# Performance work log

Hardware: AMD Instinct MI355X
Metric: run time of the kernel (lower is better)

Reference implementation:

```python
import jax, jax.numpy as jnp
import numpy as np

B, R, N, D, H, QK, K = 32, 200, 200, 128, 8, 16, 10
CLIP = 10.0  # standard POMO logit clipping


def setup_inputs() -> dict:
    key = jax.random.key(0)
    ks = jax.random.split(key, 12)
    encoded_nodes = jax.random.normal(ks[0], (B, N, D), jnp.float32)
    distance = jax.random.uniform(ks[1], (B, N, N), jnp.float32)
    current = jax.random.randint(ks[2], (B, R), 0, N)
    u = jax.random.uniform(ks[3], (B, R, N))
    ninf_mask = jnp.where(u < 0.3, -jnp.inf, 0.0).astype(jnp.float32)
    s = 0.02
    Wq = jax.random.normal(ks[4], (2 * D, H * QK), jnp.float32) * s
    Wk = jax.random.normal(ks[5], (D, H * QK), jnp.float32) * s
    Wv = jax.random.normal(ks[6], (D, H * QK), jnp.float32) * s
    Wmhc = jax.random.normal(ks[7], (H * QK, D), jnp.float32) * s
    b_mhc = jnp.zeros((D,), jnp.float32)
    W1 = jax.random.normal(ks[8], (K * D, 5 * D), jnp.float32) * s
    b1 = jnp.zeros((5 * D,), jnp.float32)
    W2 = jax.random.normal(ks[9], (5 * D, D), jnp.float32) * s
    b2 = jnp.zeros((D,), jnp.float32)
    return {"encoded_nodes": encoded_nodes, "distance": distance, "ninf_mask": ninf_mask,
            "current": current, "Wq": Wq, "Wk": Wk, "Wv": Wv, "Wmhc": Wmhc, "b_mhc": b_mhc,
            "W1": W1, "b1": b1, "W2": W2, "b2": b2}


def _search_unvisited(current, distance, ninf_mask):
    # rows of distance at current nodes: [B,R,N] (avoids B*R*N*N materialization)
    dist_f = jnp.take_along_axis(distance, current[:, :, None], axis=1)
    dist_m = jnp.where(jnp.isfinite(ninf_mask), dist_f, jnp.inf)
    neg_vals, idx = jax.lax.top_k(-dist_m, K)  # k smallest distances
    vals = -neg_vals
    return jnp.where(jnp.isinf(vals), N, idx)  # pad index N for masked-out slots


def _gather_pad0(encoded_nodes, idx):
    padded = jnp.concatenate([encoded_nodes, jnp.zeros((B, 1, D), encoded_nodes.dtype)], axis=1)
    g = jnp.take_along_axis(padded, idx.reshape(B, R * K)[:, :, None], axis=1)
    return g.reshape(B, R, K, D)


def _gather_pad_avg(a):
    # replace all-zero (pad) rows by the mean of non-zero rows within each [K,D] group
    is_zero = jnp.sum(a, axis=-1) == 0  # [B,R,K]
    cnt = jnp.maximum(jnp.sum(~is_zero, axis=-1).astype(a.dtype), 1e-9)  # [B,R]
    mean = jnp.sum(a, axis=2) / cnt[..., None]  # [B,R,D]
    return jnp.where(is_zero[..., None], mean[:, :, None, :], a)


def reference(encoded_nodes, distance, ninf_mask, current,
              Wq, Wk, Wv, Wmhc, b_mhc, W1, b1, W2, b2):
    knn = _search_unvisited(current, distance, ninf_mask)         # [B,R,K]
    a = _gather_pad0(encoded_nodes, knn)                          # [B,R,K,D]
    b = _gather_pad_avg(a)                                        # [B,R,K,D]
    h = jnp.maximum(b.reshape(B, R, K * D) @ W1 + b1, 0.0)
    unv = h @ W2 + b2                                             # [B,R,D]
    cur_emb = jnp.take_along_axis(encoded_nodes, current[:, :, None], axis=1)  # [B,R,D]
    qin = jnp.concatenate([cur_emb, unv], axis=-1)                # [B,R,2D]
    q = (qin @ Wq).reshape(B, R, H, QK).transpose(0, 2, 1, 3)     # [B,H,R,QK]
    k = (encoded_nodes @ Wk).reshape(B, N, H, QK).transpose(0, 2, 1, 3)
    v = (encoded_nodes @ Wv).reshape(B, N, H, QK).transpose(0, 2, 1, 3)
    score = jnp.einsum('bhrd,bhnd->bhrn', q, k) / jnp.sqrt(jnp.float32(QK))
    score = score + ninf_mask[:, None]                            # [B,H,R,N]
    w = jax.nn.softmax(score, axis=-1)
    out = jnp.einsum('bhrn,bhnd->bhrd', w, v)
    out = out.transpose(0, 2, 1, 3).reshape(B, R, H * QK)
    mh = out @ Wmhc + b_mhc                                       # [B,R,D]
    sh = jnp.einsum('brd,bnd->brn', mh, encoded_nodes) / jnp.sqrt(jnp.float32(D))
    logits = CLIP * jnp.tanh(sh) + ninf_mask
    return jax.nn.softmax(logits, axis=-1)                        # [B,R,N]
```

## Files before the change

kernel.cpp:

```cpp
#include <hip/hip_runtime.h>
#include <hip/hip_bf16.h>
#include <math.h>

#define Bc 32
#define Rc 200
#define Nc 200
#define Dc 128
#define Hc 8
#define QKc 16
#define Kc 10
#define BRc (Bc*Rc)

typedef __attribute__((ext_vector_type(8))) short short8;
typedef __attribute__((ext_vector_type(4))) float f32x4;
typedef unsigned long long u64;

#define GLOAD_LDS16(g, l) __builtin_amdgcn_global_load_lds( \
    (const __attribute__((address_space(1))) void*)(g), \
    (__attribute__((address_space(3))) void*)(l), 16, 0, 0)

__device__ inline void transpose_tile(const float* __restrict__ src, int lds_,
                                      __hip_bfloat16* __restrict__ dst, int ldd,
                                      int k0, int n0, float scale)
{
    __shared__ float tile[32][33];
    int tx = threadIdx.x & 31, ty = threadIdx.x >> 5;
    #pragma unroll
    for (int i = ty; i < 32; i += 8)
        tile[i][tx] = src[(size_t)(k0 + i) * lds_ + n0 + tx];
    __syncthreads();
    #pragma unroll
    for (int i = ty; i < 32; i += 8)
        dst[(size_t)(n0 + i) * ldd + k0 + tx] = __float2bfloat16(tile[tx][i] * scale);
}

__global__ __launch_bounds__(256) void prep_knn_kernel(
    const float* __restrict__ W1, const float* __restrict__ W2,
    const float* __restrict__ Wq, const float* __restrict__ Wmhc,
    const float* __restrict__ Wk, const float* __restrict__ Wv,
    const float* __restrict__ b2, const float* __restrict__ enc,
    const float* __restrict__ dist, const float* __restrict__ mask,
    const int* __restrict__ cur,
    __hip_bfloat16* __restrict__ W1t, __hip_bfloat16* __restrict__ Wkvt,
    __hip_bfloat16* __restrict__ Wmb, __hip_bfloat16* __restrict__ Wcat,
    float* __restrict__ bq, __hip_bfloat16* __restrict__ encb,
    unsigned* __restrict__ aoff, __hip_bfloat16* __restrict__ hq,
    u64* __restrict__ maskbits)
{
    int bid = blockIdx.x;
    int t = threadIdx.x;
    if (bid < 800) {
        transpose_tile(W1, 640, W1t, 1280, (bid % 40) * 32, (bid / 40) * 32, 1.f);
    } else if (bid < 816) {
        int id = bid - 800;
        transpose_tile(Wk, 128, Wkvt, 128, (id & 3) * 32, (id >> 2) * 32, 1.f);
    } else if (bid < 832) {
        int id = bid - 816;
        transpose_tile(Wv, 128, Wkvt + 128 * 128, 128, (id & 3) * 32, (id >> 2) * 32, 1.f);
    } else if (bid < 848) {
        int e = (bid - 832) * 1024 + t * 4;
        #pragma unroll
        for (int j = 0; j < 4; ++j) Wmb[e + j] = __float2bfloat16(Wmhc[e + j]);
    } else if (bid < 864) {
        int id = bid - 848;
        transpose_tile(Wq, 128, Wcat, 768, (id & 3) * 32, (id >> 2) * 32, 0.25f);
    } else if (bid < 904) {
        __shared__ float w2s[16 * 128];
        int j0 = (bid - 864) * 16;
        #pragma unroll
        for (int idx = t; idx < 16 * 128; idx += 256)
            w2s[idx] = W2[(size_t)j0 * 128 + idx];
        __syncthreads();
        int n = t & 127, half = t >> 7;
        float acc[8];
        #pragma unroll
        for (int jj = 0; jj < 8; ++jj) acc[jj] = 0.f;
        const float* wqp = Wq + (size_t)128 * 128 + n;
        #pragma unroll 8
        for (int k = 0; k < 128; ++k) {
            float wq = wqp[(size_t)k * 128];
            #pragma unroll
            for (int jj = 0; jj < 8; ++jj)
                acc[jj] = fmaf(w2s[(half * 8 + jj) * 128 + k], wq, acc[jj]);
        }
        #pragma unroll
        for (int jj = 0; jj < 8; ++jj)
            Wcat[(size_t)n * 768 + 128 + j0 + half * 8 + jj] =
                __float2bfloat16(acc[jj] * 0.25f);
    } else if (bid < 929) {
        size_t base = (size_t)(bid - 904) * 32768 + (size_t)t * 4;
        #pragma unroll 4
        for (int it = 0; it < 32; ++it) {
            size_t i = base + (size_t)it * 1024;
            float4 v = *(const float4*)(enc + i);
            encb[i + 0] = __float2bfloat16(v.x);
            encb[i + 1] = __float2bfloat16(v.y);
            encb[i + 2] = __float2bfloat16(v.z);
            encb[i + 3] = __float2bfloat16(v.w);
        }
    } else if (bid == 929) {
        __shared__ float red[128];
        int n = t & 127, half = t >> 7;
        float a0 = 0.f, a1 = 0.f;
        int kb = half * 64;
        #pragma unroll 8
        for (int k = 0; k < 64; k += 2) {
            a0 = fmaf(b2[kb + k],     Wq[(size_t)(128 + kb + k) * 128 + n], a0);
            a1 = fmaf(b2[kb + k + 1], Wq[(size_t)(128 + kb + k + 1) * 128 + n], a1);
        }
        if (half) red[n] = a0 + a1;
        __syncthreads();
        if (!half) bq[n] = (a0 + a1 + red[n]) * 0.25f;
    } else {
        int lane = t & 63, w = t >> 6;
        int br = (bid - 930) * 4 + w;
        int b = br / Rc;
        int c = cur[br];
        const float* drow = dist + ((size_t)b * Nc + c) * Nc;
        const float* mrow = mask + (size_t)br * Nc;

        float v[4];
        #pragma unroll
        for (int j = 0; j < 4; ++j) {
            int n = lane + 64 * j;
            bool allowed = false;
            float val = INFINITY;
            if (n < Nc) {
                float mv = mrow[n];
                if (!isinf(mv)) { val = drow[n]; allowed = true; }
            }
            v[j] = val;
            u64 wb = __ballot(allowed);
            if (lane == 0) maskbits[(size_t)br * 4 + j] = wb;
        }
        int idxs[Kc];
        unsigned myrow = 0;
        #pragma unroll
        for (int k = 0; k < Kc; ++k) {
            float bv = v[0]; int bn = lane;
            #pragma unroll
            for (int j = 1; j < 4; ++j) {
                if (v[j] < bv) { bv = v[j]; bn = lane + 64 * j; }
            }
            #pragma unroll
            for (int off = 32; off > 0; off >>= 1) {
                float ov = __shfl_xor(bv, off);
                int   on = __shfl_xor(bn, off);
                if (ov < bv || (ov == bv && on < bn)) { bv = ov; bn = on; }
            }
            bool pad = isinf(bv);
            idxs[k] = pad ? Nc : bn;
            if (lane == k) myrow = pad ? (unsigned)(Bc * Nc + br) : (unsigned)(b * Nc + bn);
            int oj = bn >> 6, ol = bn & 63;
            if (!pad && lane == ol) v[oj] = INFINITY;
        }
        if (lane < Kc) aoff[(size_t)br * 16 + lane] = myrow << 7;

        const float* erow = enc + ((size_t)b * Nc + c) * Dc;
        __hip_bfloat16* hrow = hq + (size_t)br * 768;
        hrow[lane]      = __float2bfloat16(erow[lane]);
        hrow[lane + 64] = __float2bfloat16(erow[lane + 64]);

        if (idxs[Kc - 1] == Nc) {
            float cnt = 0.f;
            #pragma unroll
            for (int k = 0; k < Kc; ++k) cnt += (idxs[k] < Nc) ? 1.f : 0.f;
            float icnt = 1.f / fmaxf(cnt, 1e-9f);
            #pragma unroll
            for (int half = 0; half < 2; ++half) {
                int d = lane + 64 * half;
                float sum = 0.f;
                #pragma unroll
                for (int k = 0; k < Kc; ++k) {
                    if (idxs[k] < Nc)
                        sum += enc[((size_t)b * Nc + idxs[k]) * Dc + d];
                }
                encb[((size_t)(Bc * Nc) + br) * Dc + d] = __float2bfloat16(sum * icnt);
            }
        }
    }
}

__global__ __launch_bounds__(256) void fused_gemms_kernel(
    const __hip_bfloat16* __restrict__ encb, const unsigned* __restrict__ aoff,
    const __hip_bfloat16* __restrict__ W1t, const float* __restrict__ b1,
    const __hip_bfloat16* __restrict__ Wkvt, const __hip_bfloat16* __restrict__ Wmb,
    const float* __restrict__ bmhc, const float* __restrict__ enc,
    __hip_bfloat16* __restrict__ hq, __hip_bfloat16* __restrict__ kvf,
    __hip_bfloat16* __restrict__ em, float* __restrict__ be)
{
    __shared__ short Asl[4][64 * 32];
    __shared__ short Bsl[4][64 * 32];
    int bid = blockIdx.x;
    int tid = threadIdx.x;
    int wave = tid >> 6, lane = tid & 63;
    int lrow = lane >> 2;
    int cg   = lane & 3;
    int ss   = (lane >> 3) & 3;
    int gq   = (cg - ss) & 3;
    int wm = wave >> 1, wn = wave & 1;
    int rrow = lane & 15, quad = lane >> 4;
    int srd  = (rrow >> 1) & 3;
    int strip = (wave & 1) * 32;

    if (bid < 1000) {
        int m0 = (bid / 10) * 64, n0 = (bid % 10) * 64;
        unsigned o0[Kc], o1[Kc];
        if (wave < 2) {
            const unsigned* ap0 = aoff + (size_t)(m0 + strip + lrow) * 16;
            const unsigned* ap1 = ap0 + 16 * 16;
            #pragma unroll
            for (int j = 0; j < Kc; ++j) { o0[j] = ap0[j]; o1[j] = ap1[j]; }
        }
        const short* Eb = (const short*)encb;
        const short* gB0 = (const short*)W1t + (size_t)(n0 + strip + lrow) * 1280 + gq * 8;
        const short* gB1 = gB0 + (size_t)16 * 1280;

        f32x4 acc[2][2];
        #pragma unroll
        for (int i = 0; i < 2; ++i)
            #pragma unroll
            for (int j = 0; j < 2; ++j)
                acc[i][j] = (f32x4){0.f, 0.f, 0.f, 0.f};

#define G1_STAGE(bsel, kt) do {                                                   \
            int g_ = (kt) >> 1, hh_ = ((kt) & 1) * 64;                            \
            _Pragma("unroll")                                                     \
            for (int s_ = 0; s_ < 2; ++s_) {                                      \
                if (wave < 2) {                                                   \
                    GLOAD_LDS16(Eb + o0[g_] + hh_ + s_ * 32 + gq * 8,             \
                                &Asl[((bsel) << 1) | s_][strip * 32]);            \
                    GLOAD_LDS16(Eb + o1[g_] + hh_ + s_ * 32 + gq * 8,             \
                                &Asl[((bsel) << 1) | s_][(strip + 16) * 32]);     \
                } else {                                                          \
                    GLOAD_LDS16(gB0 + (kt) * 64 + s_ * 32,                        \
                                &Bsl[((bsel) << 1) | s_][strip * 32]);            \
                    GLOAD_LDS16(gB1 + (kt) * 64 + s_ * 32,                        \
                                &Bsl[((bsel) << 1) | s_][(strip + 16) * 32]);     \
                }                                                                 \
            } } while (0)

#define G1_COMPUTE(bsel) do {                                                     \
            _Pragma("unroll")                                                     \
            for (int s_ = 0; s_ < 2; ++s_) {                                      \
                short8 afr[2], bfr[2];                                            \
                _Pragma("unroll")                                                 \
                for (int mt = 0; mt < 2; ++mt)                                    \
                    afr[mt] = *(const short8*)&Asl[((bsel) << 1) | s_]            \
                        [(wm * 32 + mt * 16 + rrow) * 32 + ((quad + srd) & 3) * 8]; \
                _Pragma("unroll")                                                 \
                for (int nt = 0; nt < 2; ++nt)                                    \
                    bfr[nt] = *(const short8*)&Bsl[((bsel) << 1) | s_]            \
                        [(wn * 32 + nt * 16 + rrow) * 32 + ((quad + srd) & 3) * 8]; \
                _Pragma("unroll")                                                 \
                for (int mt = 0; mt < 2; ++mt)                                    \
                    _Pragma("unroll")                                             \
                    for (int nt = 0; nt < 2; ++nt)                                \
                        acc[mt][nt] = __builtin_amdgcn_mfma_f32_16x16x32_bf16(    \
                            afr[mt], bfr[nt], acc[mt][nt], 0, 0, 0);              \
            } } while (0)

        G1_STAGE(0, 0);
        __syncthreads();
        #pragma unroll
        for (int kt = 0; kt < 19; ++kt) {
            G1_STAGE((kt & 1) ^ 1, kt + 1);
            G1_COMPUTE(kt & 1);
            __syncthreads();
        }
        G1_COMPUTE(1);
#undef G1_STAGE
#undef G1_COMPUTE

        #pragma unroll
        for (int mt = 0; mt < 2; ++mt)
            #pragma unroll
            for (int nt = 0; nt < 2; ++nt) {
                int n = wn * 32 + nt * 16 + rrow;
                float bv = b1[n0 + n];
                #pragma unroll
                for (int i = 0; i < 4; ++i) {
                    int m = m0 + wm * 32 + mt * 16 + quad * 4 + i;
                    float vv = fmaxf(acc[mt][nt][i] + bv, 0.f);
                    hq[(size_t)m * 768 + 128 + n0 + n] = __float2bfloat16(vv);
                }
            }
    } else if (bid < 1600) {
        const short* Bbase; __hip_bfloat16* Cout; int ldc, m0, n0;
        if (bid < 1400) {
            int id = bid - 1000;
            Bbase = (const short*)Wkvt; Cout = kvf; ldc = 256;
            m0 = (id >> 2) * 64; n0 = (id & 3) * 64;
        } else {
            int id = bid - 1400;
            Bbase = (const short*)Wmb; Cout = em; ldc = 128;
            m0 = (id >> 1) * 64; n0 = (id & 1) * 64;
        }
        const short* g0 = (wave < 2)
            ? (const short*)encb + (size_t)(m0 + strip + lrow) * 128 + gq * 8
            : Bbase + (size_t)(n0 + strip + lrow) * 128 + gq * 8;
        const short* g1 = g0 + (size_t)16 * 128;

        f32x4 acc[2][2];
        #pragma unroll
        for (int i = 0; i < 2; ++i)
            #pragma unroll
            for (int j = 0; j < 2; ++j)
                acc[i][j] = (f32x4){0.f, 0.f, 0.f, 0.f};

        #pragma unroll
        for (int s = 0; s < 4; ++s) {
            short* l0 = (wave < 2) ? &Asl[s][strip * 32] : &Bsl[s][strip * 32];
            short* l1 = (wave < 2) ? &Asl[s][(strip + 16) * 32] : &Bsl[s][(strip + 16) * 32];
            GLOAD_LDS16(g0 + s * 32, l0);
            GLOAD_LDS16(g1 + s * 32, l1);
        }
        __syncthreads();
        #pragma unroll
        for (int s = 0; s < 4; ++s) {
            short8 afr[2], bfr[2];
            #pragma unroll
            for (int mt = 0; mt < 2; ++mt)
                afr[mt] = *(const short8*)&Asl[s][(wm * 32 + mt * 16 + rrow) * 32 + ((quad + srd) & 3) * 8];
            #pragma unroll
            for (int nt = 0; nt < 2; ++nt)
                bfr[nt] = *(const short8*)&Bsl[s][(wn * 32 + nt * 16 + rrow) * 32 + ((quad + srd) & 3) * 8];
            #pragma unroll
            for (int mt = 0; mt < 2; ++mt)
                #pragma unroll
                for (int nt = 0; nt < 2; ++nt)
                    acc[mt][nt] = __builtin_amdgcn_mfma_f32_16x16x32_bf16(
                        afr[mt], bfr[nt], acc[mt][nt], 0, 0, 0);
        }
        #pragma unroll
        for (int mt = 0; mt < 2; ++mt)
            #pragma unroll
            for (int nt = 0; nt < 2; ++nt) {
                int n = wn * 32 + nt * 16 + rrow;
                #pragma unroll
                for (int i = 0; i < 4; ++i) {
                    int m = m0 + wm * 32 + mt * 16 + quad * 4 + i;
                    Cout[(size_t)m * ldc + n0 + n] = __float2bfloat16(acc[mt][nt][i]);
                }
            }
    } else {
        int i = (bid - 1600) * 256 + tid;
        if (i < Bc * Nc) {
            const float* row = enc + (size_t)i * 128;
            float acc = 0.f;
            #pragma unroll
            for (int dq = 0; dq < 32; ++dq) {
                float4 e4 = *(const float4*)(row + dq * 4);
                acc = fmaf(bmhc[dq * 4 + 0], e4.x, acc);
                acc = fmaf(bmhc[dq * 4 + 1], e4.y, acc);
                acc = fmaf(bmhc[dq * 4 + 2], e4.z, acc);
                acc = fmaf(bmhc[dq * 4 + 3], e4.w, acc);
            }
            be[i] = acc;
        }
    }
}

__global__ __launch_bounds__(256) void qgemm_kernel(
    const __hip_bfloat16* __restrict__ hq, const __hip_bfloat16* __restrict__ Wcat,
    const float* __restrict__ bq, __hip_bfloat16* __restrict__ q)
{
    __shared__ short Asl[4][64 * 32];
    __shared__ short Bsl[4][64 * 32];
    int tid = threadIdx.x;
    int wave = tid >> 6, lane = tid & 63;
    int m0 = blockIdx.y * 64, n0 = blockIdx.x * 64;
    int lrow = lane >> 2;
    int cg   = lane & 3;
    int ss   = (lane >> 3) & 3;
    int gq   = (cg - ss) & 3;
    int wm = wave >> 1, wn = wave & 1;
    int rrow = lane & 15, quad = lane >> 4;
    int srd  = (rrow >> 1) & 3;
    int strip = (wave & 1) * 32;

    const short* g0 = (wave < 2)
        ? (const short*)hq + (size_t)(m0 + strip + lrow) * 768 + gq * 8
        : (const short*)Wcat + (size_t)(n0 + strip + lrow) * 768 + gq * 8;
    const short* g1 = g0 + (size_t)16 * 768;

    f32x4 acc[2][2];
    #pragma unroll
    for (int i = 0; i < 2; ++i)
        #pragma unroll
        for (int j = 0; j < 2; ++j)
            acc[i][j] = (f32x4){0.f, 0.f, 0.f, 0.f};

#define Q_STAGE(bsel, kt) do {                                                    \
        _Pragma("unroll")                                                         \
        for (int s_ = 0; s_ < 2; ++s_) {                                          \
            short* l0_ = (wave < 2) ? &Asl[((bsel) << 1) | s_][strip * 32]        \
                                    : &Bsl[((bsel) << 1) | s_][strip * 32];       \
            short* l1_ = (wave < 2) ? &Asl[((bsel) << 1) | s_][(strip + 16) * 32] \
                                    : &Bsl[((bsel) << 1) | s_][(strip + 16) * 32];\
            GLOAD_LDS16(g0 + (kt) * 64 + s_ * 32, l0_);                           \
            GLOAD_LDS16(g1 + (kt) * 64 + s_ * 32, l1_);                           \
        } } while (0)

#define Q_COMPUTE(bsel) do {                                                      \
        _Pragma("unroll")                                                         \
        for (int s_ = 0; s_ < 2; ++s_) {                                          \
            short8 afr[2], bfr[2];                                                \
            _Pragma("unroll")                                                     \
            for (int mt = 0; mt < 2; ++mt)                                        \
                afr[mt] = *(const short8*)&Asl[((bsel) << 1) | s_]                \
                    [(wm * 32 + mt * 16 + rrow) * 32 + ((quad + srd) & 3) * 8];   \
            _Pragma("unroll")                                                     \
            for (int nt = 0; nt < 2; ++nt)                                        \
                bfr[nt] = *(const short8*)&Bsl[((bsel) << 1) | s_]                \
                    [(wn * 32 + nt * 16 + rrow) * 32 + ((quad + srd) & 3) * 8];   \
            _Pragma("unroll")                                                     \
            for (int mt = 0; mt < 2; ++mt)                                        \
                _Pragma("unroll")                                                 \
                for (int nt = 0; nt < 2; ++nt)                                    \
                    acc[mt][nt] = __builtin_amdgcn_mfma_f32_16x16x32_bf16(        \
                        afr[mt], bfr[nt], acc[mt][nt], 0, 0, 0);                  \
        } } while (0)

    Q_STAGE(0, 0);
    __syncthreads();
    #pragma unroll
    for (int kt = 0; kt < 11; ++kt) {
        Q_STAGE((kt & 1) ^ 1, kt + 1);
        Q_COMPUTE(kt & 1);
        __syncthreads();
    }
    Q_COMPUTE(1);
#undef Q_STAGE
#undef Q_COMPUTE

    #pragma unroll
    for (int mt = 0; mt < 2; ++mt) {
        #pragma unroll
        for (int nt = 0; nt < 2; ++nt) {
            int n = wn * 32 + nt * 16 + rrow;
            float bv = bq[n0 + n];
            #pragma unroll
            for (int i = 0; i < 4; ++i) {
                int m = m0 + wm * 32 + mt * 16 + quad * 4 + i;
                q[(size_t)m * 128 + n0 + n] = __float2bfloat16(acc[mt][nt][i] + bv);
            }
        }
    }
}

__global__ __launch_bounds__(256) void attn_mfma_kernel(
    const __hip_bfloat16* __restrict__ q, const __hip_bfloat16* __restrict__ kvf,
    const u64* __restrict__ maskbits, __hip_bfloat16* __restrict__ att)
{
    constexpr int RP = 208;
    constexpr int QS = 40;
    constexpr int VS = 232;
    __shared__ short Qs[RP * QS];
    __shared__ short Ks[RP * QS];
    __shared__ short Vt[16 * VS];
    __shared__ short Ps[4][16 * VS];
    __shared__ u64 smask[RP][4];

    int b = blockIdx.x >> 3, h = blockIdx.x & 7;
    int half = blockIdx.y;
    int t = threadIdx.x;
    int wave = t >> 6, lane = t & 63;
    int rrow = lane & 15, quad = lane >> 4;

    const short8 z8 = {0, 0, 0, 0, 0, 0, 0, 0};
    for (int idx = t; idx < RP * 2; idx += 256) {
        int r = idx >> 1, g = idx & 1;
        short8 qa = z8, ka = z8;
        if (r < Rc) {
            qa = *(const short8*)((const short*)q + ((size_t)(b * Rc + r)) * 128 + h * 16 + g * 8);
            ka = *(const short8*)((const short*)kvf + ((size_t)(b * Nc + r)) * 256 + h * 16 + g * 8);
        }
        *(short8*)&Qs[r * QS + g * 8] = qa;
        *(short8*)&Ks[r * QS + g * 8] = ka;
        *(short8*)&Qs[r * QS + 16 + g * 8] = z8;
        *(short8*)&Ks[r * QS + 16 + g * 8] = z8;
    }
    if (t < Rc) {
        const short* vp = (const short*)kvf + ((size_t)(b * Nc + t)) * 256 + 128 + h * 16;
        short8 v0 = *(const short8*)vp;
        short8 v1 = *(const short8*)(vp + 8);
        #pragma unroll
        for (int d = 0; d < 8; ++d) Vt[d * VS + t] = v0[d];
        #pragma unroll
        for (int d = 0; d < 8; ++d) Vt[(d + 8) * VS + t] = v1[d];
    }
    for (int idx = t; idx < 16 * 32; idx += 256) {
        int d = idx >> 5, cN = 200 + (idx & 31);
        if (cN < VS) Vt[d * VS + cN] = 0;
    }
    for (int idx = lane; idx < 16 * 16; idx += 64) {
        int rr = idx >> 4, cc = 208 + (idx & 15);
        Ps[wave][rr * VS + cc] = 0;
    }
    for (int idx = t; idx < RP * 4; idx += 256) {
        int r = idx >> 2, w = idx & 3;
        smask[r][w] = (r < Rc) ? maskbits[((size_t)b * Rc + r) * 4 + w] : ~0ull;
    }
    __syncthreads();

    int rt0 = half * 7, rt1 = half ? 13 : 7;
    for (int rt = rt0 + wave; rt < rt1; rt += 4) {
        short8 qf = *(const short8*)&Qs[(rt * 16 + rrow) * QS + quad * 8];
        f32x4 sacc[13];
        #pragma unroll
        for (int nt = 0; nt < 13; ++nt) {
            short8 kf = *(const short8*)&Ks[(nt * 16 + rrow) * QS + quad * 8];
            sacc[nt] = __builtin_amdgcn_mfma_f32_16x16x32_bf16(
                qf, kf, (f32x4){0.f, 0.f, 0.f, 0.f}, 0, 0, 0);
        }
        float inv[4];
        #pragma unroll
        for (int i = 0; i < 4; ++i) {
            int r = rt * 16 + quad * 4 + i;
            u64 wv0 = smask[r][0], wv1 = smask[r][1], wv2 = smask[r][2], wv3 = smask[r][3];
            float mx = -INFINITY;
            #pragma unroll
            for (int nt = 0; nt < 13; ++nt) {
                u64 w = (nt < 4) ? wv0 : (nt < 8) ? wv1 : (nt < 12) ? wv2 : wv3;
                int sh = ((nt & 3) << 4) + rrow;
                float s = ((w >> sh) & 1ull) ? sacc[nt][i] : -INFINITY;
                sacc[nt][i] = s;
                mx = fmaxf(mx, s);
            }
            mx = fmaxf(mx, __shfl_xor(mx, 1));
            mx = fmaxf(mx, __shfl_xor(mx, 2));
            mx = fmaxf(mx, __shfl_xor(mx, 4));
            mx = fmaxf(mx, __shfl_xor(mx, 8));
            float l = 0.f;
            #pragma unroll
            for (int nt = 0; nt < 13; ++nt) {
                float p = __expf(sacc[nt][i] - mx);
                sacc[nt][i] = p;
                l += p;
            }
            l += __shfl_xor(l, 1);
            l += __shfl_xor(l, 2);
            l += __shfl_xor(l, 4);
            l += __shfl_xor(l, 8);
            inv[i] = (l > 0.f) ? 1.f / l : 0.f;
        }
        #pragma unroll
        for (int nt = 0; nt < 13; ++nt)
            #pragma unroll
            for (int i = 0; i < 4; ++i)
                *(__hip_bfloat16*)&Ps[wave][(quad * 4 + i) * VS + nt * 16 + rrow] =
                    __float2bfloat16(sacc[nt][i]);
        f32x4 oacc = (f32x4){0.f, 0.f, 0.f, 0.f};
        #pragma unroll
        for (int kt = 0; kt < 7; ++kt) {
            short8 pf = *(const short8*)&Ps[wave][rrow * VS + kt * 32 + quad * 8];
            short8 vf = *(const short8*)&Vt[rrow * VS + kt * 32 + quad * 8];
            oacc = __builtin_amdgcn_mfma_f32_16x16x32_bf16(pf, vf, oacc, 0, 0, 0);
        }
        #pragma unroll
        for (int i = 0; i < 4; ++i) {
            int r = rt * 16 + quad * 4 + i;
            if (r < Rc)
                att[((size_t)(b * Rc + r)) * 128 + h * 16 + rrow] =
                    __float2bfloat16(oacc[i] * inv[i]);
        }
    }
}

__global__ __launch_bounds__(256) void logits_softmax_kernel(
    const __hip_bfloat16* __restrict__ att, const __hip_bfloat16* __restrict__ em,
    const float* __restrict__ be, const u64* __restrict__ maskbits,
    float* __restrict__ out)
{
    __shared__ short Asl[4][64 * 32];
    __shared__ short Bsl[4][208 * 32];
    __shared__ u64 sm[64][4];
    __shared__ float sbe[208];
    int b = blockIdx.x, m0 = blockIdx.y * 64;
    int t = threadIdx.x, wave = t >> 6, lane = t & 63;
    int lrow = lane >> 2, cg = lane & 3, ss = (lane >> 3) & 3, gq = (cg - ss) & 3;
    int rrow = lane & 15, quad = lane >> 4, srd = (rrow >> 1) & 3;

    const short* Aa = (const short*)att + ((size_t)b * Rc + m0) * 128;
    const short* Ben = (const short*)em + (size_t)b * Nc * 128;

    #pragma unroll
    for (int kc = 0; kc < 4; ++kc)
        GLOAD_LDS16(Aa + (size_t)(wave * 16 + lrow) * 128 + kc * 32 + gq * 8,
                    &Asl[kc][(wave * 16) * 32]);
    for (int cch = wave; cch < 13; cch += 4)
        #pragma unroll
        for (int kc = 0; kc < 4; ++kc)
            GLOAD_LDS16(Ben + (size_t)(cch * 16 + lrow) * 128 + kc * 32 + gq * 8,
                        &Bsl[kc][(cch * 16) * 32]);
    {
        int r = t >> 2, w = t & 3;
        sm[r][w] = (m0 + r < Rc) ? maskbits[((size_t)b * Rc + m0 + r) * 4 + w] : 0ull;
    }
    if (t < 208) sbe[t] = (t < Nc) ? be[(size_t)b * Nc + t] : 0.f;
    __syncthreads();

    short8 afr[4];
    #pragma unroll
    for (int kc = 0; kc < 4; ++kc)
        afr[kc] = *(const short8*)&Asl[kc][(wave * 16 + rrow) * 32 + ((quad + srd) & 3) * 8];

    f32x4 acc[13];
    #pragma unroll
    for (int nt = 0; nt < 13; ++nt)
        acc[nt] = (f32x4){0.f, 0.f, 0.f, 0.f};
    #pragma unroll
    for (int nt = 0; nt < 13; ++nt)
        #pragma unroll
        for (int kc = 0; kc < 4; ++kc) {
            short8 bfr = *(const short8*)
                &Bsl[kc][(nt * 16 + rrow) * 32 + ((quad + srd) & 3) * 8];
            acc[nt] = __builtin_amdgcn_mfma_f32_16x16x32_bf16(afr[kc], bfr, acc[nt], 0, 0, 0);
        }

    const float scale = 0.08838834764831843f;
    #pragma unroll
    for (int i = 0; i < 4; ++i) {
        int rloc = wave * 16 + quad * 4 + i;
        int r = m0 + rloc;
        u64 w0 = sm[rloc][0], w1 = sm[rloc][1], w2 = sm[rloc][2], w3 = sm[rloc][3];
        float vals[13];
        float mx = -INFINITY;
        #pragma unroll
        for (int nt = 0; nt < 13; ++nt) {
            u64 w = (nt < 4) ? w0 : (nt < 8) ? w1 : (nt < 12) ? w2 : w3;
            int sh = ((nt & 3) << 4) + rrow;
            float lg = -INFINITY;
            if ((w >> sh) & 1ull) {
                float y = (acc[nt][i] + sbe[nt * 16 + rrow]) * scale;
                float e = __expf(2.f * y);
                lg = 10.f * (1.f - 2.f / (e + 1.f));
            }
            vals[nt] = lg;
            mx = fmaxf(mx, lg);
        }
        mx = fmaxf(mx, __shfl_xor(mx, 1));
        mx = fmaxf(mx, __shfl_xor(mx, 2));
        mx = fmaxf(mx, __shfl_xor(mx, 4));
        mx = fmaxf(mx, __shfl_xor(mx, 8));
        float l = 0.f;
        #pragma unroll
        for (int nt = 0; nt < 13; ++nt) {
            float p = (vals[nt] == -INFINITY) ? 0.f : __expf(vals[nt] - mx);
            vals[nt] = p;
            l += p;
        }
        l += __shfl_xor(l, 1);
        l += __shfl_xor(l, 2);
        l += __shfl_xor(l, 4);
        l += __shfl_xor(l, 8);
        float inv = (l > 0.f) ? 1.f / l : 0.f;
        if (r < Rc) {
            #pragma unroll
            for (int nt = 0; nt < 13; ++nt) {
                int n = nt * 16 + rrow;
                if (n < Nc)
                    out[((size_t)b * Rc + r) * Nc + n] = vals[nt] * inv;
            }
        }
    }
}

extern "C" void kernel_launch(void* const* d_in, const int* in_sizes, int n_in,
                              void* d_out, int out_size, void* d_ws, size_t ws_size,
                              hipStream_t stream)
{
    const float* enc  = (const float*)d_in[0];
    const float* dist = (const float*)d_in[1];
    const float* mask = (const float*)d_in[2];
    const int*   cur  = (const int*)d_in[3];
    const float* Wq   = (const float*)d_in[4];
    const float* Wk   = (const float*)d_in[5];
    const float* Wv   = (const float*)d_in[6];
    const float* Wmhc = (const float*)d_in[7];
    const float* bmhc = (const float*)d_in[8];
    const float* W1   = (const float*)d_in[9];
    const float* b1   = (const float*)d_in[10];
    const float* W2   = (const float*)d_in[11];
    const float* b2   = (const float*)d_in[12];
    float* out = (float*)d_out;

    char* ws = (char*)d_ws;
    size_t off = 0;
    auto alloc = [&](size_t bytes) { char* p = ws + off; off += (bytes + 255) & ~(size_t)255; return p; };
    __hip_bfloat16* W1t  = (__hip_bfloat16*)alloc((size_t)640 * 1280 * 2);
    __hip_bfloat16* Wkvt = (__hip_bfloat16*)alloc((size_t)256 * 128 * 2);
    __hip_bfloat16* Wmb  = (__hip_bfloat16*)alloc((size_t)128 * 128 * 2);
    __hip_bfloat16* Wcat = (__hip_bfloat16*)alloc((size_t)128 * 768 * 2);
    float* bq = (float*)alloc((size_t)128 * 4);
    __hip_bfloat16* encb = (__hip_bfloat16*)alloc((size_t)(Bc * Nc + BRc + 64) * Dc * 2);
    unsigned* aoff = (unsigned*)alloc((size_t)BRc * 16 * 4);
    __hip_bfloat16* hq   = (__hip_bfloat16*)alloc((size_t)BRc * 768 * 2);
    __hip_bfloat16* q    = (__hip_bfloat16*)alloc((size_t)BRc * 128 * 2);
    __hip_bfloat16* kvf  = (__hip_bfloat16*)alloc((size_t)Bc * Nc * 256 * 2);
    __hip_bfloat16* att  = (__hip_bfloat16*)alloc((size_t)(BRc + 64) * 128 * 2);
    __hip_bfloat16* em   = (__hip_bfloat16*)alloc((size_t)(Bc * Nc + 64) * 128 * 2);
    float* be = (float*)alloc((size_t)Bc * Nc * 4);
    u64* maskbits = (u64*)alloc((size_t)BRc * 4 * 8);

    prep_knn_kernel<<<2530, 256, 0, stream>>>(
        W1, W2, Wq, Wmhc, Wk, Wv, b2, enc, dist, mask, cur,
        W1t, Wkvt, Wmb, Wcat, bq, encb, aoff, hq, maskbits);
    fused_gemms_kernel<<<1625, 256, 0, stream>>>(
        encb, aoff, W1t, b1, Wkvt, Wmb, bmhc, enc, hq, kvf, em, be);
    qgemm_kernel<<<dim3(2, BRc / 64), 256, 0, stream>>>(hq, Wcat, bq, q);
    attn_mfma_kernel<<<dim3(Bc * Hc, 2), 256, 0, stream>>>(q, kvf, maskbits, att);
    logits_softmax_kernel<<<dim3(Bc, 4), 256, 0, stream>>>(att, em, be, maskbits, out);
}
```

Before: 161.2 us.

## Widen W1 GEMM tile to 64x128 and reorder prep blocks to schedule KNN first

The first MLP GEMM now uses 64x128 output tiles instead of 64x64, so all four waves load both A and B and each wave computes a 2x4 set of MFMA tiles. This halves the number of gathered A-row loads per output column and reduces the block count, with more accumulator registers and a larger LDS buffer per block. The prep kernel is reordered so the KNN/top-k blocks get the lowest block indices and are dispatched first, ahead of the weight transposes, likely so the longer-running blocks do not form a tail.

```diff
diff --git a/kernel.cpp b/kernel.cpp
--- a/kernel.cpp
+++ b/kernel.cpp
@@ -49,71 +49,9 @@
 {
     int bid = blockIdx.x;
     int t = threadIdx.x;
-    if (bid < 800) {
-        transpose_tile(W1, 640, W1t, 1280, (bid % 40) * 32, (bid / 40) * 32, 1.f);
-    } else if (bid < 816) {
-        int id = bid - 800;
-        transpose_tile(Wk, 128, Wkvt, 128, (id & 3) * 32, (id >> 2) * 32, 1.f);
-    } else if (bid < 832) {
-        int id = bid - 816;
-        transpose_tile(Wv, 128, Wkvt + 128 * 128, 128, (id & 3) * 32, (id >> 2) * 32, 1.f);
-    } else if (bid < 848) {
-        int e = (bid - 832) * 1024 + t * 4;
-        #pragma unroll
-        for (int j = 0; j < 4; ++j) Wmb[e + j] = __float2bfloat16(Wmhc[e + j]);
-    } else if (bid < 864) {
-        int id = bid - 848;
-        transpose_tile(Wq, 128, Wcat, 768, (id & 3) * 32, (id >> 2) * 32, 0.25f);
-    } else if (bid < 904) {
-        __shared__ float w2s[16 * 128];
-        int j0 = (bid - 864) * 16;
-        #pragma unroll
-        for (int idx = t; idx < 16 * 128; idx += 256)
-            w2s[idx] = W2[(size_t)j0 * 128 + idx];
-        __syncthreads();
-        int n = t & 127, half = t >> 7;
-        float acc[8];
-        #pragma unroll
-        for (int jj = 0; jj < 8; ++jj) acc[jj] = 0.f;
-        const float* wqp = Wq + (size_t)128 * 128 + n;
-        #pragma unroll 8
-        for (int k = 0; k < 128; ++k) {
-            float wq = wqp[(size_t)k * 128];
-            #pragma unroll
-            for (int jj = 0; jj < 8; ++jj)
-                acc[jj] = fmaf(w2s[(half * 8 + jj) * 128 + k], wq, acc[jj]);
-        }
-        #pragma unroll
-        for (int jj = 0; jj < 8; ++jj)
-            Wcat[(size_t)n * 768 + 128 + j0 + half * 8 + jj] =
-                __float2bfloat16(acc[jj] * 0.25f);
-    } else if (bid < 929) {
-        size_t base = (size_t)(bid - 904) * 32768 + (size_t)t * 4;
-        #pragma unroll 4
-        for (int it = 0; it < 32; ++it) {
-            size_t i = base + (size_t)it * 1024;
-            float4 v = *(const float4*)(enc + i);
-            encb[i + 0] = __float2bfloat16(v.x);
-            encb[i + 1] = __float2bfloat16(v.y);
-            encb[i + 2] = __float2bfloat16(v.z);
-            encb[i + 3] = __float2bfloat16(v.w);
-        }
-    } else if (bid == 929) {
-        __shared__ float red[128];
-        int n = t & 127, half = t >> 7;
-        float a0 = 0.f, a1 = 0.f;
-        int kb = half * 64;
-        #pragma unroll 8
-        for (int k = 0; k < 64; k += 2) {
-            a0 = fmaf(b2[kb + k],     Wq[(size_t)(128 + kb + k) * 128 + n], a0);
-            a1 = fmaf(b2[kb + k + 1], Wq[(size_t)(128 + kb + k + 1) * 128 + n], a1);
-        }
-        if (half) red[n] = a0 + a1;
-        __syncthreads();
-        if (!half) bq[n] = (a0 + a1 + red[n]) * 0.25f;
-    } else {
+    if (bid < 1600) {
         int lane = t & 63, w = t >> 6;
-        int br = (bid - 930) * 4 + w;
+        int br = bid * 4 + w;
         int b = br / Rc;
         int c = cur[br];
         const float* drow = dist + ((size_t)b * Nc + c) * Nc;
@@ -178,6 +116,69 @@
                 encb[((size_t)(Bc * Nc) + br) * Dc + d] = __float2bfloat16(sum * icnt);
             }
         }
+    } else if (bid < 2400) {
+        int id = bid - 1600;
+        transpose_tile(W1, 640, W1t, 1280, (id % 40) * 32, (id / 40) * 32, 1.f);
+    } else if (bid < 2416) {
+        int id = bid - 2400;
+        transpose_tile(Wk, 128, Wkvt, 128, (id & 3) * 32, (id >> 2) * 32, 1.f);
+    } else if (bid < 2432) {
+        int id = bid - 2416;
+        transpose_tile(Wv, 128, Wkvt + 128 * 128, 128, (id & 3) * 32, (id >> 2) * 32, 1.f);
+    } else if (bid < 2448) {
+        int e = (bid - 2432) * 1024 + t * 4;
+        #pragma unroll
+        for (int j = 0; j < 4; ++j) Wmb[e + j] = __float2bfloat16(Wmhc[e + j]);
+    } else if (bid < 2464) {
+        int id = bid - 2448;
+        transpose_tile(Wq, 128, Wcat, 768, (id & 3) * 32, (id >> 2) * 32, 0.25f);
+    } else if (bid < 2504) {
+        __shared__ float w2s[16 * 128];
+        int j0 = (bid - 2464) * 16;
+        #pragma unroll
+        for (int idx = t; idx < 16 * 128; idx += 256)
+            w2s[idx] = W2[(size_t)j0 * 128 + idx];
+        __syncthreads();
+        int n = t & 127, half = t >> 7;
+        float acc[8];
+        #pragma unroll
+        for (int jj = 0; jj < 8; ++jj) acc[jj] = 0.f;
+        const float* wqp = Wq + (size_t)128 * 128 + n;
+        #pragma unroll 8
+        for (int k = 0; k < 128; ++k) {
+            float wq = wqp[(size_t)k * 128];
+            #pragma unroll
+            for (int jj = 0; jj < 8; ++jj)
+                acc[jj] = fmaf(w2s[(half * 8 + jj) * 128 + k], wq, acc[jj]);
+        }
+        #pragma unroll
+        for (int jj = 0; jj < 8; ++jj)
+            Wcat[(size_t)n * 768 + 128 + j0 + half * 8 + jj] =
+                __float2bfloat16(acc[jj] * 0.25f);
+    } else if (bid < 2529) {
+        size_t base = (size_t)(bid - 2504) * 32768 + (size_t)t * 4;
+        #pragma unroll 4
+        for (int it = 0; it < 32; ++it) {
+            size_t i = base + (size_t)it * 1024;
+            float4 v = *(const float4*)(enc + i);
+            encb[i + 0] = __float2bfloat16(v.x);
+            encb[i + 1] = __float2bfloat16(v.y);
+            encb[i + 2] = __float2bfloat16(v.z);
+            encb[i + 3] = __float2bfloat16(v.w);
+        }
+    } else {
+        __shared__ float red[128];
+        int n = t & 127, half = t >> 7;
+        float a0 = 0.f, a1 = 0.f;
+        int kb = half * 64;
+        #pragma unroll 8
+        for (int k = 0; k < 64; k += 2) {
+            a0 = fmaf(b2[kb + k],     Wq[(size_t)(128 + kb + k) * 128 + n], a0);
+            a1 = fmaf(b2[kb + k + 1], Wq[(size_t)(128 + kb + k + 1) * 128 + n], a1);
+        }
+        if (half) red[n] = a0 + a1;
+        __syncthreads();
+        if (!half) bq[n] = (a0 + a1 + red[n]) * 0.25f;
     }
 }
 
@@ -190,7 +191,7 @@
     __hip_bfloat16* __restrict__ em, float* __restrict__ be)
 {
     __shared__ short Asl[4][64 * 32];
-    __shared__ short Bsl[4][64 * 32];
+    __shared__ short Bsl[4][128 * 32];
     int bid = blockIdx.x;
     int tid = threadIdx.x;
     int wave = tid >> 6, lane = tid & 63;
@@ -203,59 +204,53 @@
     int srd  = (rrow >> 1) & 3;
     int strip = (wave & 1) * 32;
 
-    if (bid < 1000) {
-        int m0 = (bid / 10) * 64, n0 = (bid % 10) * 64;
-        unsigned o0[Kc], o1[Kc];
-        if (wave < 2) {
-            const unsigned* ap0 = aoff + (size_t)(m0 + strip + lrow) * 16;
-            const unsigned* ap1 = ap0 + 16 * 16;
-            #pragma unroll
-            for (int j = 0; j < Kc; ++j) { o0[j] = ap0[j]; o1[j] = ap1[j]; }
-        }
-        const short* Eb = (const short*)encb;
-        const short* gB0 = (const short*)W1t + (size_t)(n0 + strip + lrow) * 1280 + gq * 8;
+    if (bid < 500) {
+        int m0 = (bid / 5) * 64, n0 = (bid % 5) * 128;
+        unsigned oA[Kc];
+        {
+            const unsigned* ap = aoff + (size_t)(m0 + wave * 16 + lrow) * 16;
+            #pragma unroll
+            for (int j = 0; j < Kc; ++j) oA[j] = ap[j];
+        }
+        const short* Eb  = (const short*)encb;
+        const short* gB0 = (const short*)W1t + (size_t)(n0 + wave * 32 + lrow) * 1280 + gq * 8;
         const short* gB1 = gB0 + (size_t)16 * 1280;
 
-        f32x4 acc[2][2];
+        f32x4 acc[2][4];
         #pragma unroll
         for (int i = 0; i < 2; ++i)
             #pragma unroll
-            for (int j = 0; j < 2; ++j)
+            for (int j = 0; j < 4; ++j)
                 acc[i][j] = (f32x4){0.f, 0.f, 0.f, 0.f};
 
 #define G1_STAGE(bsel, kt) do {                                                   \
             int g_ = (kt) >> 1, hh_ = ((kt) & 1) * 64;                            \
             _Pragma("unroll")                                                     \
             for (int s_ = 0; s_ < 2; ++s_) {                                      \
-                if (wave < 2) {                                                   \
-                    GLOAD_LDS16(Eb + o0[g_] + hh_ + s_ * 32 + gq * 8,             \
-                                &Asl[((bsel) << 1) | s_][strip * 32]);            \
-                    GLOAD_LDS16(Eb + o1[g_] + hh_ + s_ * 32 + gq * 8,             \
-                                &Asl[((bsel) << 1) | s_][(strip + 16) * 32]);     \
-                } else {                                                          \
-                    GLOAD_LDS16(gB0 + (kt) * 64 + s_ * 32,                        \
-                                &Bsl[((bsel) << 1) | s_][strip * 32]);            \
-                    GLOAD_LDS16(gB1 + (kt) * 64 + s_ * 32,                        \
-                                &Bsl[((bsel) << 1) | s_][(strip + 16) * 32]);     \
-                }                                                                 \
+                GLOAD_LDS16(Eb + oA[g_] + hh_ + s_ * 32 + gq * 8,                 \
+                            &Asl[((bsel) << 1) | s_][(wave * 16) * 32]);          \
+                GLOAD_LDS16(gB0 + (kt) * 64 + s_ * 32,                            \
+                            &Bsl[((bsel) << 1) | s_][(wave * 32) * 32]);          \
+                GLOAD_LDS16(gB1 + (kt) * 64 + s_ * 32,                            \
+                            &Bsl[((bsel) << 1) | s_][(wave * 32 + 16) * 32]);     \
             } } while (0)
 
 #define G1_COMPUTE(bsel) do {                                                     \
             _Pragma("unroll")                                                     \
             for (int s_ = 0; s_ < 2; ++s_) {                                      \
-                short8 afr[2], bfr[2];                                            \
+                short8 afr[2], bfr[4];                                            \
                 _Pragma("unroll")                                                 \
                 for (int mt = 0; mt < 2; ++mt)                                    \
                     afr[mt] = *(const short8*)&Asl[((bsel) << 1) | s_]            \
                         [(wm * 32 + mt * 16 + rrow) * 32 + ((quad + srd) & 3) * 8]; \
                 _Pragma("unroll")                                                 \
-                for (int nt = 0; nt < 2; ++nt)                                    \
+                for (int nt = 0; nt < 4; ++nt)                                    \
                     bfr[nt] = *(const short8*)&Bsl[((bsel) << 1) | s_]            \
-                        [(wn * 32 + nt * 16 + rrow) * 32 + ((quad + srd) & 3) * 8]; \
+                        [(wn * 64 + nt * 16 + rrow) * 32 + ((quad + srd) & 3) * 8]; \
                 _Pragma("unroll")                                                 \
                 for (int mt = 0; mt < 2; ++mt)                                    \
                     _Pragma("unroll")                                             \
-                    for (int nt = 0; nt < 2; ++nt)                                \
+                    for (int nt = 0; nt < 4; ++nt)                                \
                         acc[mt][nt] = __builtin_amdgcn_mfma_f32_16x16x32_bf16(    \
                             afr[mt], bfr[nt], acc[mt][nt], 0, 0, 0);              \
             } } while (0)
@@ -275,8 +270,8 @@
         #pragma unroll
         for (int mt = 0; mt < 2; ++mt)
             #pragma unroll
-            for (int nt = 0; nt < 2; ++nt) {
-                int n = wn * 32 + nt * 16 + rrow;
+            for (int nt = 0; nt < 4; ++nt) {
+                int n = wn * 64 + nt * 16 + rrow;
                 float bv = b1[n0 + n];
                 #pragma unroll
                 for (int i = 0; i < 4; ++i) {
@@ -285,14 +280,14 @@
                     hq[(size_t)m * 768 + 128 + n0 + n] = __float2bfloat16(vv);
                 }
             }
-    } else if (bid < 1600) {
+    } else if (bid < 1100) {
         const short* Bbase; __hip_bfloat16* Cout; int ldc, m0, n0;
-        if (bid < 1400) {
-            int id = bid - 1000;
+        if (bid < 900) {
+            int id = bid - 500;
             Bbase = (const short*)Wkvt; Cout = kvf; ldc = 256;
             m0 = (id >> 2) * 64; n0 = (id & 3) * 64;
         } else {
-            int id = bid - 1400;
+            int id = bid - 900;
             Bbase = (const short*)Wmb; Cout = em; ldc = 128;
             m0 = (id >> 1) * 64; n0 = (id & 1) * 64;
         }
@@ -344,7 +339,7 @@
                 }
             }
     } else {
-        int i = (bid - 1600) * 256 + tid;
+        int i = (bid - 1100) * 256 + tid;
         if (i < Bc * Nc) {
             const float* row = enc + (size_t)i * 128;
             float acc = 0.f;
@@ -707,7 +702,7 @@
     prep_knn_kernel<<<2530, 256, 0, stream>>>(
         W1, W2, Wq, Wmhc, Wk, Wv, b2, enc, dist, mask, cur,
         W1t, Wkvt, Wmb, Wcat, bq, encb, aoff, hq, maskbits);
-    fused_gemms_kernel<<<1625, 256, 0, stream>>>(
+    fused_gemms_kernel<<<1125, 256, 0, stream>>>(
         encb, aoff, W1t, b1, Wkvt, Wmb, bmhc, enc, hq, kvf, em, be);
     qgemm_kernel<<<dim3(2, BRc / 64), 256, 0, stream>>>(hq, Wcat, bq, q);
     attn_mfma_kernel<<<dim3(Bc * Hc, 2), 256, 0, stream>>>(q, kvf, maskbits, att);
```

After: 162.2 us. Within noise of the previous version (+0.6%).
